# Optimization experiments

Measured on AMD Instinct MI355X. Metric: run time of the kernel, lower is better.

Reference implementation:

```python
import jax, jax.numpy as jnp
import numpy as np

PARTS = [list(range(0, 17)), list(range(17, 22)), list(range(22, 27)),
         list(range(27, 36)), list(range(36, 42)), list(range(42, 48)),
         list(range(48, 68))]
NUM_PARTS = len(PARTS)
V_JOINTS = max(max(p) for p in PARTS) + 1  # 68
# joint -> part index (same as get_corr_joints)
JOINTS = np.zeros((V_JOINTS,), dtype=np.int32)
for j, part in enumerate(PARTS):
    for i in part:
        JOINTS[i] = j
BN_EPS = 1e-5


def setup_inputs() -> dict:
    key = jax.random.key(0)
    k0, k1, k2 = jax.random.split(key, 3)
    N, C, T, V = 512, 1024, 1, V_JOINTS
    x = jax.random.normal(k0, (N, C, T, V), dtype=jnp.float32)
    conv1_w = jax.random.normal(k1, (C // 4, C), dtype=jnp.float32) * 0.02  # 1x1 conv C->C/4
    conv1_b = jnp.zeros((C // 4,), dtype=jnp.float32)
    conv2_w = jax.random.normal(k2, (2,), dtype=jnp.float32) * 0.5  # 1x1 conv 2->1
    conv2_b = jnp.zeros((), dtype=jnp.float32)
    bn_gamma = jnp.ones((C,), dtype=jnp.float32)
    bn_beta = jnp.zeros((C,), dtype=jnp.float32)
    return {"x": x, "conv1_w": conv1_w, "conv1_b": conv1_b,
            "conv2_w": conv2_w, "conv2_b": conv2_b,
            "bn_gamma": bn_gamma, "bn_beta": bn_beta}


def _forward(x, conv1_w, conv1_b, conv2_w, conv2_b, bn_gamma, bn_beta):
    N, C, T, V = x.shape  # T must be 1 (required by original .view)
    joints = jnp.asarray(JOINTS)
    P = NUM_PARTS
    # part-wise mean pool over joints: (V,P) normalized one-hot
    M = jax.nn.one_hot(joints, P, dtype=x.dtype)
    M = M / jnp.sum(M, axis=0, keepdims=True)
    x_parts = jnp.einsum('nctv,vp->nctp', x, M)            # (N,C,T,P)
    # conv1: 1x1, C -> C/4
    h = jnp.einsum('nctp,oc->notp', x_parts, conv1_w) + conv1_b[None, :, None, None]
    x_cap = jnp.mean(h, axis=1, keepdims=True)             # channel avg pool
    x_cmp = jnp.max(h, axis=1, keepdims=True)              # channel max pool
    # conv2: 1x1, 2 -> 1 (cat order is (avg, max))
    att = conv2_w[0] * x_cap + conv2_w[1] * x_cmp + conv2_b  # (N,1,T,P)
    att = jnp.broadcast_to(att, (N, C, T, P)).reshape(N, C, P)
    att = jax.nn.softmax(att, axis=-1)                     # softmax over parts
    # scatter part attention back to joints
    att_j = att[:, :, joints][:, :, None, :]               # (N,C,1,V)
    y = x * att_j
    # BatchNorm2d (training mode: batch stats over N,T,V per channel)
    mean = jnp.mean(y, axis=(0, 2, 3), keepdims=True)
    var = jnp.var(y, axis=(0, 2, 3), keepdims=True)
    y_bn = (y - mean) * jax.lax.rsqrt(var + BN_EPS)
    y_bn = y_bn * bn_gamma[None, :, None, None] + bn_beta[None, :, None, None]
    return jax.nn.relu(y_bn + x)


def reference(x, conv1_w, conv1_b, conv2_w, conv2_b, bn_gamma, bn_beta):
    return _forward(x, conv1_w, conv1_b, conv2_w, conv2_b, bn_gamma, bn_beta)
```

## Files before the change

kernel.cpp:

```cpp
#include <hip/hip_runtime.h>

#define NN 512
#define CC 1024
#define OO 256
#define VV 68
#define PP 7
#define NC (NN*CC)
#define NV_CNT 34816.0f

typedef float floatx4 __attribute__((ext_vector_type(4)));

__device__ __forceinline__ int part_of(int v){
  return (v>=17)+(v>=22)+(v>=27)+(v>=36)+(v>=42)+(v>=48);
}

__global__ __launch_bounds__(256) void k0_prep(const float* __restrict__ w1,
    float* __restrict__ w1p){
  int g = blockIdx.x*256 + threadIdx.x;
  int o = g >> 8, cb = g & 255;
  float4 v = ((const float4*)w1)[g];
  ((float4*)w1p)[cb*256 + o] = v;
}

__global__ __launch_bounds__(256) void k12_att(const float* __restrict__ x,
    const float* __restrict__ w1p, const float* __restrict__ b1,
    const float* __restrict__ w2, const float* __restrict__ b2,
    float* __restrict__ att, float* __restrict__ partial){
  int n = blockIdx.x;
  int t = threadIdx.x;

  __shared__ float stg[68*129];
  __shared__ float4 sSf4[PP*256];
  __shared__ float red_s[4][PP], red_m[4][PP], pre[PP], att_s[PP];
  float* sSl  = (float*)sSf4;
  float* hred = stg;
  float* sqt  = stg + 2048;

  int row  = t & 127;
  int half = t >> 7;

  float q2r[8][4];
  #pragma unroll
  for (int j=0;j<8;j++){
    q2r[j][0]=0.f; q2r[j][1]=0.f; q2r[j][2]=0.f; q2r[j][3]=0.f;
  }

  const float4* xb = (const float4*)(x + (size_t)n*CC*VV);
  #pragma unroll
  for (int j=0;j<8;j++){
    const float4* src = xb + j*2176;
    #pragma unroll
    for (int k=0;k<9;k++){
      int g = k*256 + t;
      if (k==8 && t>=128) break;
      float4 v4 = src[g];
      int rr = g/17, q = g - rr*17;
      stg[(q*4+0)*129 + rr] = v4.x;
      stg[(q*4+1)*129 + rr] = v4.y;
      stg[(q*4+2)*129 + rr] = v4.z;
      stg[(q*4+3)*129 + rr] = v4.w;
    }
    __syncthreads();
    if (half==0){
      float s[3] = {0.f,0.f,0.f};
      #pragma unroll
      for (int v=0; v<27; v++){
        int p = part_of(v);
        float e = stg[v*129 + row];
        s[p] += e;
        q2r[j][p] = fmaf(e, e, q2r[j][p]);
      }
      #pragma unroll
      for (int p=0;p<3;p++) sSl[p*1024 + j*128 + row] = s[p];
    } else {
      float s[4] = {0.f,0.f,0.f,0.f};
      #pragma unroll
      for (int v=27; v<68; v++){
        int p = part_of(v) - 3;
        float e = stg[v*129 + row];
        s[p] += e;
        q2r[j][p] = fmaf(e, e, q2r[j][p]);
      }
      #pragma unroll
      for (int p=0;p<4;p++) sSl[(p+3)*1024 + j*128 + row] = s[p];
    }
    __syncthreads();
  }

  int oh = t & 31, ch = t >> 5;
  float acc[8][PP];
  #pragma unroll
  for (int k=0;k<8;k++)
    #pragma unroll
    for (int p=0;p<PP;p++) acc[k][p] = 0.f;

  const float4* wp = (const float4*)w1p;
  for (int i=0;i<32;i++){
    int gcb = ch*32 + i;
    const float4* wrow = wp + (size_t)gcb*256 + oh;
    float4 w[8];
    #pragma unroll
    for (int k=0;k<8;k++) w[k] = wrow[32*k];
    #pragma unroll
    for (int p=0;p<PP;p++){
      float4 sv = sSf4[p*256 + gcb];
      #pragma unroll
      for (int k=0;k<8;k++){
        acc[k][p] = fmaf(w[k].x, sv.x, acc[k][p]);
        acc[k][p] = fmaf(w[k].y, sv.y, acc[k][p]);
        acc[k][p] = fmaf(w[k].z, sv.z, acc[k][p]);
        acc[k][p] = fmaf(w[k].w, sv.w, acc[k][p]);
      }
    }
  }

  const float inv_cnt[PP] = {1.f/17.f,1.f/5.f,1.f/5.f,1.f/9.f,1.f/6.f,1.f/6.f,1.f/20.f};
  float bo = b1[t];
  float h[PP];
  #pragma unroll
  for (int p=0;p<PP;p++){
    __syncthreads();
    #pragma unroll
    for (int k=0;k<8;k++) hred[ch*256 + k*32 + oh] = acc[k][p];
    __syncthreads();
    float hs = 0.f;
    #pragma unroll
    for (int c8=0;c8<8;c8++) hs += hred[c8*256 + t];
    h[p] = fmaf(hs, inv_cnt[p], bo);
  }

  int lane = t & 63, wid = t >> 6;
  #pragma unroll
  for (int p=0;p<PP;p++){
    float sm = h[p], mx = h[p];
    #pragma unroll
    for (int off=32; off>0; off>>=1){
      sm += __shfl_down(sm, off, 64);
      mx = fmaxf(mx, __shfl_down(mx, off, 64));
    }
    if (lane==0){ red_s[wid][p]=sm; red_m[wid][p]=mx; }
  }
  __syncthreads();
  if (t < PP){
    int p = t;
    float sm = red_s[0][p]+red_s[1][p]+red_s[2][p]+red_s[3][p];
    float mx = fmaxf(fmaxf(red_m[0][p],red_m[1][p]),
                     fmaxf(red_m[2][p],red_m[3][p]));
    pre[p] = w2[0]*(sm*(1.f/(float)OO)) + w2[1]*mx + b2[0];
  }
  __syncthreads();
  if (t == 0){
    float m = pre[0];
    #pragma unroll
    for (int p=1;p<PP;p++) m = fmaxf(m, pre[p]);
    float e[PP], sum=0.f;
    #pragma unroll
    for (int p=0;p<PP;p++){ e[p] = expf(pre[p]-m); sum += e[p]; }
    float inv = 1.f/sum;
    #pragma unroll
    for (int p=0;p<PP;p++){
      float a = e[p]*inv;
      att_s[p] = a;
      att[n*PP+p] = a;
    }
  }
  __syncthreads();

  float a[PP];
  #pragma unroll
  for (int p=0;p<PP;p++) a[p] = att_s[p];

  #pragma unroll
  for (int jj=0;jj<4;jj++){
    int c = jj*256 + t;
    float sm = 0.f;
    #pragma unroll
    for (int p=0;p<PP;p++) sm = fmaf(a[p], sSl[p*1024 + c], sm);
    partial[n*2048 + c] = sm;
  }

  if (half==1){
    #pragma unroll
    for (int j=0;j<8;j++){
      float sq = 0.f;
      #pragma unroll
      for (int p=0;p<4;p++){
        float ap = a[p+3];
        sq = fmaf(ap*ap, q2r[j][p], sq);
      }
      sqt[j*128 + row] = sq;
    }
  }
  __syncthreads();
  if (half==0){
    #pragma unroll
    for (int j=0;j<8;j++){
      float sq = sqt[j*128 + row];
      #pragma unroll
      for (int p=0;p<3;p++){
        float ap = a[p];
        sq = fmaf(ap*ap, q2r[j][p], sq);
      }
      partial[n*2048 + 1024 + j*128 + row] = sq;
    }
  }
}

__global__ __launch_bounds__(256) void k3b_finalize(const float* __restrict__ partial,
    const float* __restrict__ gamma, const float* __restrict__ beta,
    float* __restrict__ scsh){
  __shared__ float rs[8][32], rq[8][32];
  int cl = threadIdx.x & 31, grp = threadIdx.x >> 5;
  int c = blockIdx.x*32 + cl;
  float sm=0.f, sq=0.f;
  for (int i=0;i<64;i++){
    int n = grp*64 + i;
    sm += partial[n*2048 + c];
    sq += partial[n*2048 + 1024 + c];
  }
  rs[grp][cl] = sm; rq[grp][cl] = sq;
  __syncthreads();
  if (threadIdx.x < 32){
    float tsm=0.f, tsq=0.f;
    #pragma unroll
    for (int g=0; g<8; g++){ tsm += rs[g][threadIdx.x]; tsq += rq[g][threadIdx.x]; }
    int cc = blockIdx.x*32 + threadIdx.x;
    float mean = tsm * (1.0f/NV_CNT);
    float var  = tsq * (1.0f/NV_CNT) - mean*mean;
    float rstd = rsqrtf(var + 1e-5f);
    float sc = gamma[cc]*rstd;
    scsh[cc]        = sc;
    scsh[1024 + cc] = beta[cc] - mean*sc;
  }
}

__global__ __launch_bounds__(256) void k4_out(const float* __restrict__ x,
    const float* __restrict__ att, const float* __restrict__ scsh,
    float* __restrict__ out){
  int f = blockIdx.x*256 + threadIdx.x;
  int n = blockIdx.x / 68;
  __shared__ float s_att[PP];
  if (threadIdx.x < PP) s_att[threadIdx.x] = att[n*PP + threadIdx.x];
  __syncthreads();
  int r = f/17;
  int q = f - r*17;
  int v0 = q*4;
  int c = r & (CC-1);
  float4 xv = ((const float4*)x)[f];
  float sc = scsh[c];
  float sh = scsh[1024 + c];
  float vals[4];
  #pragma unroll
  for (int j=0;j<4;j++){
    int p = part_of(v0 + j);
    float a = s_att[p];
    float e = (j==0)?xv.x:(j==1)?xv.y:(j==2)?xv.z:xv.w;
    vals[j] = fmaxf(fmaf(e, fmaf(a, sc, 1.0f), sh), 0.0f);
  }
  floatx4 ov; ov.x=vals[0]; ov.y=vals[1]; ov.z=vals[2]; ov.w=vals[3];
  __builtin_nontemporal_store(ov, ((floatx4*)out) + f);
}

extern "C" void kernel_launch(void* const* d_in, const int* in_sizes, int n_in,
                              void* d_out, int out_size, void* d_ws, size_t ws_size,
                              hipStream_t stream) {
  const float* x     = (const float*)d_in[0];
  const float* w1    = (const float*)d_in[1];
  const float* b1    = (const float*)d_in[2];
  const float* w2    = (const float*)d_in[3];
  const float* b2    = (const float*)d_in[4];
  const float* gamma = (const float*)d_in[5];
  const float* beta  = (const float*)d_in[6];
  float* out = (float*)d_out;

  float* w1p     = (float*)d_ws;
  float* partial = w1p + OO*CC;
  float* scsh    = partial + NN*2048;
  float* att     = scsh + 2048;

  k0_prep     <<<256,         256, 0, stream>>>(w1, w1p);
  k12_att     <<<NN,          256, 0, stream>>>(x, w1p, b1, w2, b2, att, partial);
  k3b_finalize<<<32,          256, 0, stream>>>(partial, gamma, beta, scsh);
  k4_out      <<<(NC*17)/256, 256, 0, stream>>>(x, att, scsh, out);
}
```

Before: 315.0 us.

## Double k12_att block to 512 threads, splitting part sums across four thread groups

```diff
diff --git a/kernel.cpp b/kernel.cpp
--- a/kernel.cpp
+++ b/kernel.cpp
@@ -22,7 +22,7 @@
   ((float4*)w1p)[cb*256 + o] = v;
 }
 
-__global__ __launch_bounds__(256) void k12_att(const float* __restrict__ x,
+__global__ __launch_bounds__(512, 4) void k12_att(const float* __restrict__ x,
     const float* __restrict__ w1p, const float* __restrict__ b1,
     const float* __restrict__ w2, const float* __restrict__ b2,
     float* __restrict__ att, float* __restrict__ partial){
@@ -34,25 +34,23 @@
   __shared__ float red_s[4][PP], red_m[4][PP], pre[PP], att_s[PP];
   float* sSl  = (float*)sSf4;
   float* hred = stg;
-  float* sqt  = stg + 2048;
+  float* sqt  = stg + 4096;
 
   int row  = t & 127;
-  int half = t >> 7;
-
-  float q2r[8][4];
-  #pragma unroll
-  for (int j=0;j<8;j++){
-    q2r[j][0]=0.f; q2r[j][1]=0.f; q2r[j][2]=0.f; q2r[j][3]=0.f;
-  }
+  int quad = t >> 7;
+
+  float q2r[8][2];
+  #pragma unroll
+  for (int j=0;j<8;j++){ q2r[j][0]=0.f; q2r[j][1]=0.f; }
 
   const float4* xb = (const float4*)(x + (size_t)n*CC*VV);
   #pragma unroll
   for (int j=0;j<8;j++){
     const float4* src = xb + j*2176;
     #pragma unroll
-    for (int k=0;k<9;k++){
-      int g = k*256 + t;
-      if (k==8 && t>=128) break;
+    for (int k=0;k<5;k++){
+      int g = k*512 + t;
+      if (k==4 && t>=128) break;
       float4 v4 = src[g];
       int rr = g/17, q = g - rr*17;
       stg[(q*4+0)*129 + rr] = v4.x;
@@ -61,28 +59,56 @@
       stg[(q*4+3)*129 + rr] = v4.w;
     }
     __syncthreads();
-    if (half==0){
-      float s[3] = {0.f,0.f,0.f};
-      #pragma unroll
-      for (int v=0; v<27; v++){
-        int p = part_of(v);
-        float e = stg[v*129 + row];
-        s[p] += e;
-        q2r[j][p] = fmaf(e, e, q2r[j][p]);
-      }
-      #pragma unroll
-      for (int p=0;p<3;p++) sSl[p*1024 + j*128 + row] = s[p];
+    if (quad==0){
+      float s0 = 0.f;
+      #pragma unroll
+      for (int v=0; v<17; v++){
+        float e = stg[v*129 + row];
+        s0 += e; q2r[j][0] = fmaf(e, e, q2r[j][0]);
+      }
+      sSl[0*1024 + j*128 + row] = s0;
+    } else if (quad==1){
+      float s1=0.f, s2=0.f;
+      #pragma unroll
+      for (int v=17; v<22; v++){
+        float e = stg[v*129 + row];
+        s1 += e; q2r[j][0] = fmaf(e, e, q2r[j][0]);
+      }
+      #pragma unroll
+      for (int v=22; v<27; v++){
+        float e = stg[v*129 + row];
+        s2 += e; q2r[j][1] = fmaf(e, e, q2r[j][1]);
+      }
+      sSl[1*1024 + j*128 + row] = s1;
+      sSl[2*1024 + j*128 + row] = s2;
+    } else if (quad==2){
+      float s3=0.f, s4=0.f;
+      #pragma unroll
+      for (int v=27; v<36; v++){
+        float e = stg[v*129 + row];
+        s3 += e; q2r[j][0] = fmaf(e, e, q2r[j][0]);
+      }
+      #pragma unroll
+      for (int v=36; v<42; v++){
+        float e = stg[v*129 + row];
+        s4 += e; q2r[j][1] = fmaf(e, e, q2r[j][1]);
+      }
+      sSl[3*1024 + j*128 + row] = s3;
+      sSl[4*1024 + j*128 + row] = s4;
     } else {
-      float s[4] = {0.f,0.f,0.f,0.f};
-      #pragma unroll
-      for (int v=27; v<68; v++){
-        int p = part_of(v) - 3;
-        float e = stg[v*129 + row];
-        s[p] += e;
-        q2r[j][p] = fmaf(e, e, q2r[j][p]);
-      }
-      #pragma unroll
-      for (int p=0;p<4;p++) sSl[(p+3)*1024 + j*128 + row] = s[p];
+      float s5=0.f, s6=0.f;
+      #pragma unroll
+      for (int v=42; v<48; v++){
+        float e = stg[v*129 + row];
+        s5 += e; q2r[j][0] = fmaf(e, e, q2r[j][0]);
+      }
+      #pragma unroll
+      for (int v=48; v<68; v++){
+        float e = stg[v*129 + row];
+        s6 += e; q2r[j][1] = fmaf(e, e, q2r[j][1]);
+      }
+      sSl[5*1024 + j*128 + row] = s5;
+      sSl[6*1024 + j*128 + row] = s6;
     }
     __syncthreads();
   }
@@ -95,8 +121,9 @@
     for (int p=0;p<PP;p++) acc[k][p] = 0.f;
 
   const float4* wp = (const float4*)w1p;
-  for (int i=0;i<32;i++){
-    int gcb = ch*32 + i;
+  #pragma unroll 2
+  for (int i=0;i<16;i++){
+    int gcb = ch*16 + i;
     const float4* wrow = wp + (size_t)gcb*256 + oh;
     float4 w[8];
     #pragma unroll
@@ -115,7 +142,7 @@
   }
 
   const float inv_cnt[PP] = {1.f/17.f,1.f/5.f,1.f/5.f,1.f/9.f,1.f/6.f,1.f/6.f,1.f/20.f};
-  float bo = b1[t];
+  float bo = (t < OO) ? b1[t] : 0.f;
   float h[PP];
   #pragma unroll
   for (int p=0;p<PP;p++){
@@ -123,22 +150,26 @@
     #pragma unroll
     for (int k=0;k<8;k++) hred[ch*256 + k*32 + oh] = acc[k][p];
     __syncthreads();
-    float hs = 0.f;
-    #pragma unroll
-    for (int c8=0;c8<8;c8++) hs += hred[c8*256 + t];
-    h[p] = fmaf(hs, inv_cnt[p], bo);
+    if (t < OO){
+      float hs = 0.f;
+      #pragma unroll
+      for (int c16=0;c16<16;c16++) hs += hred[c16*256 + t];
+      h[p] = fmaf(hs, inv_cnt[p], bo);
+    }
   }
 
   int lane = t & 63, wid = t >> 6;
-  #pragma unroll
-  for (int p=0;p<PP;p++){
-    float sm = h[p], mx = h[p];
-    #pragma unroll
-    for (int off=32; off>0; off>>=1){
-      sm += __shfl_down(sm, off, 64);
-      mx = fmaxf(mx, __shfl_down(mx, off, 64));
-    }
-    if (lane==0){ red_s[wid][p]=sm; red_m[wid][p]=mx; }
+  if (t < OO){
+    #pragma unroll
+    for (int p=0;p<PP;p++){
+      float sm = h[p], mx = h[p];
+      #pragma unroll
+      for (int off=32; off>0; off>>=1){
+        sm += __shfl_down(sm, off, 64);
+        mx = fmaxf(mx, __shfl_down(mx, off, 64));
+      }
+      if (lane==0){ red_s[wid][p]=sm; red_m[wid][p]=mx; }
+    }
   }
   __syncthreads();
   if (t < PP){
@@ -171,37 +202,32 @@
   for (int p=0;p<PP;p++) a[p] = att_s[p];
 
   #pragma unroll
-  for (int jj=0;jj<4;jj++){
-    int c = jj*256 + t;
+  for (int jj=0;jj<2;jj++){
+    int c = jj*512 + t;
     float sm = 0.f;
     #pragma unroll
     for (int p=0;p<PP;p++) sm = fmaf(a[p], sSl[p*1024 + c], sm);
     partial[n*2048 + c] = sm;
   }
 
-  if (half==1){
+  if (quad>0){
+    int pA = (quad==1)?1:(quad==2)?3:5;
+    int pB = pA + 1;
+    float aA = a[pA]*a[pA], aB = a[pB]*a[pB];
     #pragma unroll
     for (int j=0;j<8;j++){
-      float sq = 0.f;
-      #pragma unroll
-      for (int p=0;p<4;p++){
-        float ap = a[p+3];
-        sq = fmaf(ap*ap, q2r[j][p], sq);
-      }
-      sqt[j*128 + row] = sq;
-    }
-  }
-  __syncthreads();
-  if (half==0){
+      sqt[(quad-1)*1024 + j*128 + row] = aA*q2r[j][0] + aB*q2r[j][1];
+    }
+  }
+  __syncthreads();
+  if (quad==0){
+    float a0 = a[0]*a[0];
     #pragma unroll
     for (int j=0;j<8;j++){
-      float sq = sqt[j*128 + row];
-      #pragma unroll
-      for (int p=0;p<3;p++){
-        float ap = a[p];
-        sq = fmaf(ap*ap, q2r[j][p], sq);
-      }
-      partial[n*2048 + 1024 + j*128 + row] = sq;
+      int c = j*128 + row;
+      float sq = a0*q2r[j][0]
+               + sqt[0*1024 + c] + sqt[1*1024 + c] + sqt[2*1024 + c];
+      partial[n*2048 + 1024 + c] = sq;
     }
   }
 }
@@ -279,7 +305,7 @@
   float* att     = scsh + 2048;
 
   k0_prep     <<<256,         256, 0, stream>>>(w1, w1p);
-  k12_att     <<<NN,          256, 0, stream>>>(x, w1p, b1, w2, b2, att, partial);
+  k12_att     <<<NN,          512, 0, stream>>>(x, w1p, b1, w2, b2, att, partial);
   k3b_finalize<<<32,          256, 0, stream>>>(partial, gamma, beta, scsh);
   k4_out      <<<(NC*17)/256, 256, 0, stream>>>(x, att, scsh, out);
 }
```

New measurement: 353.1 us. +12.1%, slower.
